# Optimization experiments

Hardware: AMD Instinct MI355X
Metric: run time of the kernel (lower is better)

The kernel has to match this reference:

```python
import jax, jax.numpy as jnp
import numpy as np

B = 65536
LATENT = 256
POSE_DIM, SHAPE_DIM, ROT_DIM, TRANS_DIM = 15, 10, 3, 3
N_JOINTS = 16  # MANO kinematic tree (wrist + 3 per finger x 5)
PARENTS = (-1, 0, 1, 2, 0, 4, 5, 0, 7, 8, 0, 10, 11, 0, 13, 14)


def setup_inputs() -> dict:
    key = jax.random.key(0)
    ks = jax.random.split(key, 13)
    f32 = jnp.float32
    inp = {
        'z_left': jax.random.normal(ks[0], (B, LATENT), dtype=f32),
        'z_right': jax.random.normal(ks[1], (B, LATENT), dtype=f32),
        # MLP params (Linear(256,512) -> ReLU -> Linear(512,256) -> ReLU -> Linear(256,31))
        'W1': jax.random.normal(ks[2], (LATENT, 512), dtype=f32) * 0.02,
        'b1': jnp.zeros((512,), dtype=f32),
        'W2': jax.random.normal(ks[3], (512, 256), dtype=f32) * 0.02,
        'b2': jnp.zeros((256,), dtype=f32),
        'W3': jax.random.normal(ks[4], (256, 31), dtype=f32) * 0.02,
        'b3': jnp.zeros((31,), dtype=f32),
        # MANO model parameters
        'J_template': jax.random.normal(ks[5], (N_JOINTS, 3), dtype=f32) * 0.05,
        'shape_dirs': jax.random.normal(ks[6], (N_JOINTS, 3, SHAPE_DIM), dtype=f32) * 0.01,
        'hands_components': jax.random.normal(ks[7], (POSE_DIM, 45), dtype=f32) * 0.1,  # PCA -> 15 joints axis-angle
        'hands_mean': jax.random.normal(ks[8], (45,), dtype=f32) * 0.1,
    }
    return inp


def rodrigues(r):
    """Axis-angle [..., 3] -> rotation matrices [..., 3, 3]."""
    theta = jnp.sqrt(jnp.sum(r * r, axis=-1, keepdims=True) + 1e-12)  # [...,1]
    k = r / theta
    kx, ky, kz = k[..., 0], k[..., 1], k[..., 2]
    z = jnp.zeros_like(kx)
    K = jnp.stack([z, -kz, ky, kz, z, -kx, -ky, kx, z], axis=-1)
    K = K.reshape(r.shape[:-1] + (3, 3))
    ct = jnp.cos(theta)[..., None]
    st = jnp.sin(theta)[..., None]
    I = jnp.eye(3, dtype=r.dtype)
    return I + st * K + (1.0 - ct) * (K @ K)


def _decode(z, W1, b1, W2, b2, W3, b3, J_template, shape_dirs, hands_components, hands_mean, is_right):
    # small MLP -> MANO params
    h = jax.nn.relu(z @ W1 + b1)
    h = jax.nn.relu(h @ W2 + b2)
    p = h @ W3 + b3                                    # [B,31]
    pose = p[:, :POSE_DIM]                             # [B,15] PCA coeffs
    shape = p[:, POSE_DIM:POSE_DIM + SHAPE_DIM]        # [B,10]
    rot = p[:, 25:28]                                  # global axis-angle
    trans = p[:, 28:31]

    # shape blend on joint template
    J = J_template[None] + jnp.einsum('jkd,bd->bjk', shape_dirs, shape)  # [B,16,3]
    if not is_right:
        J = J * jnp.asarray([-1.0, 1.0, 1.0], dtype=z.dtype)  # mirror for left hand

    # PCA pose -> per-joint axis-angle -> rotations
    full_pose = hands_mean[None] + pose @ hands_components   # [B,45]
    aa = full_pose.reshape(-1, 15, 3)
    R_global = rodrigues(rot)            # [B,3,3]
    R_local = rodrigues(aa)              # [B,15,3,3]
    R = jnp.concatenate([R_global[:, None], R_local], axis=1)  # [B,16,3,3]

    # batched kinematic chain (fixed 16-joint tree)
    Rw = [R[:, 0]]
    t = [J[:, 0]]
    for i in range(1, N_JOINTS):
        par = PARENTS[i]
        Rw.append(jnp.einsum('bij,bjk->bik', Rw[par], R[:, i]))
        t.append(jnp.einsum('bij,bj->bi', Rw[par], J[:, i] - J[:, par]) + t[par])
    joints = jnp.stack(t, axis=1) + trans[:, None, :]   # [B,16,3]
    return joints


def reference(z_left, z_right, W1, b1, W2, b2, W3, b3, J_template, shape_dirs, hands_components, hands_mean):
    joints_left = _decode(z_left, W1, b1, W2, b2, W3, b3, J_template, shape_dirs, hands_components, hands_mean, is_right=False)
    joints_right = _decode(z_right, W1, b1, W2, b2, W3, b3, J_template, shape_dirs, hands_components, hands_mean, is_right=True)
    return (joints_left, joints_right)
```

## Files before the change

kernel.cpp:

```cpp
#include <hip/hip_runtime.h>
#include <hip/hip_bf16.h>

typedef __attribute__((ext_vector_type(8))) short short8;
typedef __attribute__((ext_vector_type(4))) float f32x4;
typedef unsigned short ushort_t;

#define MFMA16(a,b,c) __builtin_amdgcn_mfma_f32_16x16x32_bf16((a),(b),(c),0,0,0)

__device__ __forceinline__ ushort_t f2bf(float x){
  unsigned int u = __builtin_bit_cast(unsigned int, x);
  unsigned int r = (u + 0x7FFFu + ((u >> 16) & 1u)) >> 16;
  return (ushort_t)r;
}
__device__ __forceinline__ float bf2f(ushort_t h){
  unsigned int u = ((unsigned int)h) << 16;
  return __builtin_bit_cast(float, u);
}

__device__ __forceinline__ void mat3mul(float* C, const float* A, const float* B){
  #pragma unroll
  for (int i = 0; i < 3; i++)
    #pragma unroll
    for (int k = 0; k < 3; k++)
      C[i*3+k] = A[i*3+0]*B[0*3+k] + A[i*3+1]*B[1*3+k] + A[i*3+2]*B[2*3+k];
}
__device__ __forceinline__ void rotp(float* o, const float* A, float x, float y, float z, const float* t){
  o[0] = A[0]*x + A[1]*y + A[2]*z + t[0];
  o[1] = A[3]*x + A[4]*y + A[5]*z + t[1];
  o[2] = A[6]*x + A[7]*y + A[8]*z + t[2];
}

__global__ __launch_bounds__(64) void poison_kernel(float* out, float val){
  if (threadIdx.x == 0 && blockIdx.x == 0) out[0] = val;
}

__global__ __launch_bounds__(256) void preconv_kernel(
    const float* __restrict__ W1, const float* __restrict__ W2, const float* __restrict__ W3,
    ushort_t* __restrict__ W1h, ushort_t* __restrict__ W1l,
    ushort_t* __restrict__ W2h, ushort_t* __restrict__ W2l,
    ushort_t* __restrict__ W3h, ushort_t* __restrict__ W3l)
{
  const int idx = blockIdx.x * 256 + threadIdx.x;
  {
    int j = idx & 7, l = (idx >> 3) & 63, kk = (idx >> 9) & 7, nt = idx >> 12;
    int k = kk*32 + (l >> 4)*8 + j, n = nt*16 + (l & 15);
    float w = W1[k*512 + n];
    ushort_t hi = f2bf(w);
    W1h[idx] = hi; W1l[idx] = f2bf(w - bf2f(hi));
  }
  {
    int j = idx & 7, l = (idx >> 3) & 63, kk = (idx >> 9) & 15, nt = idx >> 13;
    int k = kk*32 + (l >> 4)*8 + j, n = nt*16 + (l & 15);
    float w = W2[k*256 + n];
    ushort_t hi = f2bf(w);
    W2h[idx] = hi; W2l[idx] = f2bf(w - bf2f(hi));
  }
  if (idx < 16384){
    int j = idx & 7, l = (idx >> 3) & 63, kk = (idx >> 9) & 7, nt = idx >> 12;
    int k = kk*32 + (l >> 4)*8 + j, n = nt*16 + (l & 15);
    float w = (nt < 2 && n < 31) ? W3[k*31 + n] : 0.f;
    ushort_t hi = f2bf(w);
    W3h[idx] = hi; W3l[idx] = f2bf(w - bf2f(hi));
  }
}

__global__ __launch_bounds__(256, 3) void fused_kernel(
    const float* __restrict__ zL, const float* __restrict__ zR,
    const ushort_t* __restrict__ W1h, const ushort_t* __restrict__ W1l,
    const ushort_t* __restrict__ W2h, const ushort_t* __restrict__ W2l,
    const ushort_t* __restrict__ W3h, const ushort_t* __restrict__ W3l,
    const float* __restrict__ b1, const float* __restrict__ b2, const float* __restrict__ b3,
    const float* __restrict__ Jt, const float* __restrict__ sd,
    const float* __restrict__ hc, const float* __restrict__ hm,
    float* __restrict__ out)
{
  __shared__ ushort_t regA[2*32*264];
  __shared__ ushort_t regB[2*32*72];
  __shared__ float    plbuf[32*33];
  ushort_t* regAhi = regA;
  ushort_t* regAlo = regA + 32*264;
  ushort_t* regBhi = regB;
  ushort_t* regBlo = regB + 32*72;

  const int tid  = threadIdx.x;
  const int lane = tid & 63;
  const int w    = tid >> 6;
  const int lo   = lane & 15;
  const int g    = lane >> 4;
  const int m0   = blockIdx.x * 32;
  const bool right = (m0 >= 65536);
  const float* zsrc = right ? (zR + (size_t)(m0 - 65536) * 256)
                            : (zL + (size_t)m0 * 256);

  #pragma unroll
  for (int i = 0; i < 8; i++){
    int e = i*1024 + tid*4;
    float4 v = *(const float4*)(zsrc + e);
    int r = e >> 8, c = e & 255;
    ushort_t* dh = &regAhi[r*264 + c];
    ushort_t* dl = &regAlo[r*264 + c];
    float vv[4] = {v.x, v.y, v.z, v.w};
    #pragma unroll
    for (int q = 0; q < 4; q++){
      ushort_t hi = f2bf(vv[q]);
      dh[q] = hi; dl[q] = f2bf(vv[q] - bf2f(hi));
    }
  }
  __syncthreads();

  f32x4 accL2[2][4];
  #pragma unroll
  for (int a = 0; a < 2; a++)
    #pragma unroll
    for (int b = 0; b < 4; b++)
      accL2[a][b] = (f32x4){0.f,0.f,0.f,0.f};

  for (int c = 0; c < 8; c++){
    {
      const int nt = c*4 + w;
      short8 bh[8], bl[8];
      #pragma unroll
      for (int kk = 0; kk < 8; kk++){
        bh[kk] = *(const short8*)(W1h + (size_t)(nt*8 + kk)*512 + lane*8);
        bl[kk] = *(const short8*)(W1l + (size_t)(nt*8 + kk)*512 + lane*8);
      }
      const float bias = b1[nt*16 + lo];
      #pragma unroll
      for (int rt = 0; rt < 2; rt++){
        f32x4 ahh = (f32x4){0.f,0.f,0.f,0.f};
        f32x4 ahl = (f32x4){0.f,0.f,0.f,0.f};
        f32x4 alh = (f32x4){0.f,0.f,0.f,0.f};
        #pragma unroll
        for (int kk = 0; kk < 8; kk++){
          short8 ah = *(const short8*)&regAhi[(rt*16 + lo)*264 + kk*32 + g*8];
          short8 al = *(const short8*)&regAlo[(rt*16 + lo)*264 + kk*32 + g*8];
          ahh = MFMA16(ah, bh[kk], ahh);
          ahl = MFMA16(ah, bl[kk], ahl);
          alh = MFMA16(al, bh[kk], alh);
        }
        #pragma unroll
        for (int i = 0; i < 4; i++){
          float v = fmaxf(ahh[i] + ahl[i] + alh[i] + bias, 0.f);
          ushort_t hi = f2bf(v);
          const int ro = (rt*16 + g*4 + i)*72 + w*16 + lo;
          regBhi[ro] = hi; regBlo[ro] = f2bf(v - bf2f(hi));
        }
      }
    }
    __syncthreads();
    {
      #pragma unroll
      for (int x = 0; x < 2; x++){
        short8 b2h[4], b2l[4];
        #pragma unroll
        for (int q = 0; q < 4; q++){
          b2h[q] = *(const short8*)(W2h + (size_t)((w*4+q)*16 + c*2 + x)*512 + lane*8);
          b2l[q] = *(const short8*)(W2l + (size_t)((w*4+q)*16 + c*2 + x)*512 + lane*8);
        }
        #pragma unroll
        for (int rt = 0; rt < 2; rt++){
          short8 ah = *(const short8*)&regBhi[(rt*16 + lo)*72 + x*32 + g*8];
          short8 al = *(const short8*)&regBlo[(rt*16 + lo)*72 + x*32 + g*8];
          #pragma unroll
          for (int q = 0; q < 4; q++){
            accL2[rt][q] = MFMA16(ah, b2h[q], accL2[rt][q]);
            accL2[rt][q] = MFMA16(ah, b2l[q], accL2[rt][q]);
            accL2[rt][q] = MFMA16(al, b2h[q], accL2[rt][q]);
          }
        }
      }
    }
    __syncthreads();
  }

  #pragma unroll
  for (int rt = 0; rt < 2; rt++){
    #pragma unroll
    for (int q = 0; q < 4; q++){
      const int col = w*64 + q*16 + lo;
      const float bias = b2[col];
      #pragma unroll
      for (int i = 0; i < 4; i++){
        float v = fmaxf(accL2[rt][q][i] + bias, 0.f);
        ushort_t hi = f2bf(v);
        const int ro = (rt*16 + g*4 + i)*264 + col;
        regAhi[ro] = hi; regAlo[ro] = f2bf(v - bf2f(hi));
      }
    }
  }
  __syncthreads();

  {
    const int rw = w & 1, nn = w >> 1;
    f32x4 ahh = (f32x4){0.f,0.f,0.f,0.f};
    f32x4 ahl = (f32x4){0.f,0.f,0.f,0.f};
    f32x4 alh = (f32x4){0.f,0.f,0.f,0.f};
    #pragma unroll
    for (int kk = 0; kk < 8; kk++){
      short8 ah = *(const short8*)&regAhi[(rw*16 + lo)*264 + kk*32 + g*8];
      short8 al = *(const short8*)&regAlo[(rw*16 + lo)*264 + kk*32 + g*8];
      short8 bh = *(const short8*)(W3h + (size_t)(nn*8 + kk)*512 + lane*8);
      short8 bl = *(const short8*)(W3l + (size_t)(nn*8 + kk)*512 + lane*8);
      ahh = MFMA16(ah, bh, ahh);
      ahl = MFMA16(ah, bl, ahl);
      alh = MFMA16(al, bh, alh);
    }
    const int col = nn*16 + lo;
    const float bias = (col < 31) ? b3[col] : 0.f;
    #pragma unroll
    for (int i = 0; i < 4; i++)
      plbuf[(rw*16 + g*4 + i)*33 + col] = ahh[i] + ahl[i] + alh[i] + bias;
  }
  __syncthreads();
  const float* pl = plbuf;

  if (tid < 32){
    const int r = tid;
    float p15[15];
    #pragma unroll
    for (int d = 0; d < 15; d++) p15[d] = pl[r*33 + d];
    float sh[10];
    #pragma unroll
    for (int d = 0; d < 10; d++) sh[d] = pl[r*33 + 15 + d];
    const float trx = pl[r*33+28], tr_y = pl[r*33+29], trz = pl[r*33+30];

    float J[16][3];
    #pragma unroll
    for (int jj = 0; jj < 16; jj++){
      #pragma unroll
      for (int k2 = 0; k2 < 3; k2++){
        float v = Jt[jj*3 + k2];
        #pragma unroll
        for (int d = 0; d < 10; d++) v = fmaf(sd[(jj*3 + k2)*10 + d], sh[d], v);
        J[jj][k2] = v;
      }
    }
    if (!right){
      #pragma unroll
      for (int jj = 0; jj < 16; jj++) J[jj][0] = -J[jj][0];
    }

    auto rod = [](float ax, float ay, float az, float* R){
      float th = sqrtf(ax*ax + ay*ay + az*az + 1e-12f);
      float inv = 1.0f / th;
      float kx = ax*inv, ky = ay*inv, kz = az*inv;
      float st = __sinf(th), ct = __cosf(th);
      float omc = 1.0f - ct;
      R[0] = ct + omc*kx*kx;      R[1] = omc*kx*ky - st*kz;  R[2] = omc*kx*kz + st*ky;
      R[3] = omc*kx*ky + st*kz;   R[4] = ct + omc*ky*ky;     R[5] = omc*ky*kz - st*kx;
      R[6] = omc*kx*kz - st*ky;   R[7] = omc*ky*kz + st*kx;  R[8] = ct + omc*kz*kz;
    };
    auto axis_rod = [&](int j, float* R){
      const int base = 3*(j-1);
      float s0 = hm[base+0], s1 = hm[base+1], s2 = hm[base+2];
      #pragma unroll
      for (int d = 0; d < 15; d++){
        float pv = p15[d];
        s0 = fmaf(pv, hc[d*45 + base+0], s0);
        s1 = fmaf(pv, hc[d*45 + base+1], s1);
        s2 = fmaf(pv, hc[d*45 + base+2], s2);
      }
      rod(s0, s1, s2, R);
    };

    float R0[9];
    rod(pl[r*33+25], pl[r*33+26], pl[r*33+27], R0);

    const size_t ob = (right ? (size_t)3145728 : (size_t)0)
                    + (size_t)(m0 - (right ? 65536 : 0) + r) * 48;
    float t0[3] = {J[0][0], J[0][1], J[0][2]};
    out[ob+0] = t0[0]+trx; out[ob+1] = t0[1]+tr_y; out[ob+2] = t0[2]+trz;
    #pragma unroll
    for (int f = 0; f < 5; f++){
      const int i1 = 3*f+1, i2 = 3*f+2, i3 = 3*f+3;
      float R1[9], R2[9], Rw1[9], Rw2[9], t1[3], t2[3], t3[3];
      axis_rod(i1, R1);
      axis_rod(i2, R2);
      mat3mul(Rw1, R0, R1);
      rotp(t1, R0,  J[i1][0]-J[0][0],  J[i1][1]-J[0][1],  J[i1][2]-J[0][2],  t0);
      mat3mul(Rw2, Rw1, R2);
      rotp(t2, Rw1, J[i2][0]-J[i1][0], J[i2][1]-J[i1][1], J[i2][2]-J[i1][2], t1);
      rotp(t3, Rw2, J[i3][0]-J[i2][0], J[i3][1]-J[i2][1], J[i3][2]-J[i2][2], t2);
      out[ob + i1*3+0] = t1[0]+trx; out[ob + i1*3+1] = t1[1]+tr_y; out[ob + i1*3+2] = t1[2]+trz;
      out[ob + i2*3+0] = t2[0]+trx; out[ob + i2*3+1] = t2[1]+tr_y; out[ob + i2*3+2] = t2[2]+trz;
      out[ob + i3*3+0] = t3[0]+trx; out[ob + i3*3+1] = t3[1]+tr_y; out[ob + i3*3+2] = t3[2]+trz;
    }
  }
}

extern "C" void kernel_launch(void* const* d_in, const int* in_sizes, int n_in,
                              void* d_out, int out_size, void* d_ws, size_t ws_size,
                              hipStream_t stream) {
  const float* zL = (const float*)d_in[0];
  const float* zR = (const float*)d_in[1];
  const float* W1 = (const float*)d_in[2];
  const float* b1 = (const float*)d_in[3];
  const float* W2 = (const float*)d_in[4];
  const float* b2 = (const float*)d_in[5];
  const float* W3 = (const float*)d_in[6];
  const float* b3 = (const float*)d_in[7];
  const float* Jt = (const float*)d_in[8];
  const float* sd = (const float*)d_in[9];
  const float* hc = (const float*)d_in[10];
  const float* hm = (const float*)d_in[11];

  float* out = (float*)d_out;

  if (ws_size < 1114112){
    poison_kernel<<<1, 64, 0, stream>>>(out, 20480.f);
    return;
  }

  ushort_t* W1h = (ushort_t*)d_ws;
  ushort_t* W1l = W1h + 131072;
  ushort_t* W2h = W1l + 131072;
  ushort_t* W2l = W2h + 131072;
  ushort_t* W3h = W2l + 131072;
  ushort_t* W3l = W3h + 16384;

  preconv_kernel<<<512, 256, 0, stream>>>(W1, W2, W3, W1h, W1l, W2h, W2l, W3h, W3l);
  fused_kernel<<<4096, 256, 0, stream>>>(zL, zR, W1h, W1l, W2h, W2l, W3h, W3l,
                                         b1, b2, b3, Jt, sd, hc, hm, out);
}
```

Baseline: 269.5 us.

## Widen layer-1 chunks to halve barriers and hoist A fragments into registers

The fused MLP now processes layer 1 in 4 chunks of 128 hidden units instead of 8 chunks of 64. Each wave computes two 16-column tiles per chunk and keeps the layer-1 input A fragments in registers, reused across both tiles. The intermediate LDS buffer grows to hold 128 columns, and launch bounds drop from 3 to 2 blocks per SM to give the compiler more registers. This halves the number of __syncthreads pairs and cuts redundant LDS reads of the input, at the cost of lower occupancy and more LDS per block.

```diff
diff --git a/kernel.cpp b/kernel.cpp
--- a/kernel.cpp
+++ b/kernel.cpp
@@ -64,7 +64,7 @@
   }
 }
 
-__global__ __launch_bounds__(256, 3) void fused_kernel(
+__global__ __launch_bounds__(256, 2) void fused_kernel(
     const float* __restrict__ zL, const float* __restrict__ zR,
     const ushort_t* __restrict__ W1h, const ushort_t* __restrict__ W1l,
     const ushort_t* __restrict__ W2h, const ushort_t* __restrict__ W2l,
@@ -74,13 +74,13 @@
     const float* __restrict__ hc, const float* __restrict__ hm,
     float* __restrict__ out)
 {
-  __shared__ ushort_t regA[2*32*264];
-  __shared__ ushort_t regB[2*32*72];
-  __shared__ float    plbuf[32*33];
+  __shared__ __attribute__((aligned(16))) ushort_t regA[2*32*264];
+  __shared__ __attribute__((aligned(16))) ushort_t regB[2*32*136];
+  __shared__ __attribute__((aligned(16))) float    plbuf[32*33];
   ushort_t* regAhi = regA;
   ushort_t* regAlo = regA + 32*264;
   ushort_t* regBhi = regB;
-  ushort_t* regBlo = regB + 32*72;
+  ushort_t* regBlo = regB + 32*136;
 
   const int tid  = threadIdx.x;
   const int lane = tid & 63;
@@ -115,58 +115,62 @@
     for (int b = 0; b < 4; b++)
       accL2[a][b] = (f32x4){0.f,0.f,0.f,0.f};
 
-  for (int c = 0; c < 8; c++){
-    {
-      const int nt = c*4 + w;
-      short8 bh[8], bl[8];
+  #pragma unroll
+  for (int cc = 0; cc < 4; cc++){
+    #pragma unroll
+    for (int rt = 0; rt < 2; rt++){
+      short8 ah[8], al[8];
       #pragma unroll
       for (int kk = 0; kk < 8; kk++){
-        bh[kk] = *(const short8*)(W1h + (size_t)(nt*8 + kk)*512 + lane*8);
-        bl[kk] = *(const short8*)(W1l + (size_t)(nt*8 + kk)*512 + lane*8);
-      }
-      const float bias = b1[nt*16 + lo];
-      #pragma unroll
-      for (int rt = 0; rt < 2; rt++){
+        ah[kk] = *(const short8*)&regAhi[(rt*16 + lo)*264 + kk*32 + g*8];
+        al[kk] = *(const short8*)&regAlo[(rt*16 + lo)*264 + kk*32 + g*8];
+      }
+      #pragma unroll
+      for (int t = 0; t < 2; t++){
+        const int nt = cc*8 + w*2 + t;
+        short8 bh[8], bl[8];
+        #pragma unroll
+        for (int kk = 0; kk < 8; kk++){
+          bh[kk] = *(const short8*)(W1h + (size_t)(nt*8 + kk)*512 + lane*8);
+          bl[kk] = *(const short8*)(W1l + (size_t)(nt*8 + kk)*512 + lane*8);
+        }
+        const float bias = b1[nt*16 + lo];
         f32x4 ahh = (f32x4){0.f,0.f,0.f,0.f};
         f32x4 ahl = (f32x4){0.f,0.f,0.f,0.f};
         f32x4 alh = (f32x4){0.f,0.f,0.f,0.f};
         #pragma unroll
         for (int kk = 0; kk < 8; kk++){
-          short8 ah = *(const short8*)&regAhi[(rt*16 + lo)*264 + kk*32 + g*8];
-          short8 al = *(const short8*)&regAlo[(rt*16 + lo)*264 + kk*32 + g*8];
-          ahh = MFMA16(ah, bh[kk], ahh);
-          ahl = MFMA16(ah, bl[kk], ahl);
-          alh = MFMA16(al, bh[kk], alh);
+          ahh = MFMA16(ah[kk], bh[kk], ahh);
+          ahl = MFMA16(ah[kk], bl[kk], ahl);
+          alh = MFMA16(al[kk], bh[kk], alh);
         }
         #pragma unroll
         for (int i = 0; i < 4; i++){
           float v = fmaxf(ahh[i] + ahl[i] + alh[i] + bias, 0.f);
           ushort_t hi = f2bf(v);
-          const int ro = (rt*16 + g*4 + i)*72 + w*16 + lo;
+          const int ro = (rt*16 + g*4 + i)*136 + (w*2 + t)*16 + lo;
           regBhi[ro] = hi; regBlo[ro] = f2bf(v - bf2f(hi));
         }
       }
     }
     __syncthreads();
-    {
-      #pragma unroll
-      for (int x = 0; x < 2; x++){
-        short8 b2h[4], b2l[4];
+    #pragma unroll
+    for (int x = 0; x < 4; x++){
+      short8 b2h[4], b2l[4];
+      #pragma unroll
+      for (int q = 0; q < 4; q++){
+        b2h[q] = *(const short8*)(W2h + (size_t)((w*4+q)*16 + cc*4 + x)*512 + lane*8);
+        b2l[q] = *(const short8*)(W2l + (size_t)((w*4+q)*16 + cc*4 + x)*512 + lane*8);
+      }
+      #pragma unroll
+      for (int rt = 0; rt < 2; rt++){
+        short8 ah = *(const short8*)&regBhi[(rt*16 + lo)*136 + x*32 + g*8];
+        short8 al = *(const short8*)&regBlo[(rt*16 + lo)*136 + x*32 + g*8];
         #pragma unroll
         for (int q = 0; q < 4; q++){
-          b2h[q] = *(const short8*)(W2h + (size_t)((w*4+q)*16 + c*2 + x)*512 + lane*8);
-          b2l[q] = *(const short8*)(W2l + (size_t)((w*4+q)*16 + c*2 + x)*512 + lane*8);
-        }
-        #pragma unroll
-        for (int rt = 0; rt < 2; rt++){
-          short8 ah = *(const short8*)&regBhi[(rt*16 + lo)*72 + x*32 + g*8];
-          short8 al = *(const short8*)&regBlo[(rt*16 + lo)*72 + x*32 + g*8];
-          #pragma unroll
-          for (int q = 0; q < 4; q++){
-            accL2[rt][q] = MFMA16(ah, b2h[q], accL2[rt][q]);
-            accL2[rt][q] = MFMA16(ah, b2l[q], accL2[rt][q]);
-            accL2[rt][q] = MFMA16(al, b2h[q], accL2[rt][q]);
-          }
+          accL2[rt][q] = MFMA16(ah, b2h[q], accL2[rt][q]);
+          accL2[rt][q] = MFMA16(ah, b2l[q], accL2[rt][q]);
+          accL2[rt][q] = MFMA16(al, b2h[q], accL2[rt][q]);
         }
       }
     }
```

After: 367.0 us. 1.36x slower.
